# Kernel optimization log

Measured on AMD Instinct MI355X. Metric: run time of the kernel, lower is better.

The kernel has to match this reference:

```python
import jax, jax.numpy as jnp
import numpy as np

B, S, D = 2, 2048, 1024
H, DK, DV = 16, 64, 64
EPS = 1e-5
SQRT_DK = float(np.sqrt(DK))


def setup_inputs() -> dict:
    key = jax.random.key(0)
    ks = jax.random.split(key, 8)
    sc = 0.02
    return {
        "x": jax.random.normal(ks[0], (B, S, D), jnp.float32),
        "Wk": jax.random.normal(ks[1], (D, H * DK), jnp.float32) * sc,
        "bk": jnp.zeros((H * DK,), jnp.float32),
        "Wq": jax.random.normal(ks[2], (D, H * DK), jnp.float32) * sc,
        "bq": jnp.zeros((H * DK,), jnp.float32),
        "Wv": jax.random.normal(ks[3], (D, H * DV), jnp.float32) * sc,
        "bv": jnp.zeros((H * DV,), jnp.float32),
        "Wo": jax.random.normal(ks[4], (H * DV, D), jnp.float32) * sc,
        "bo": jnp.zeros((D,), jnp.float32),
        "gamma": jnp.ones((D,), jnp.float32),
        "beta": jnp.zeros((D,), jnp.float32),
    }


def reference(x, Wk, bk, Wq, bq, Wv, bv, Wo, bo, gamma, beta):
    b, s, d = x.shape
    # NOTE: original torch code reshapes (B, S, H*dk) directly to (B, H, S, dk)
    # without a transpose; we replicate that exact (non-standard) reshape.
    keys = (x @ Wk + bk).reshape(b, H, s, DK)
    queries = (x @ Wq + bq).reshape(b, H, s, DK)
    values = (x @ Wv + bv).reshape(b, H, s, DV)

    scores = jnp.einsum('bhqd,bhkd->bhqk', queries, keys) / SQRT_DK
    causal_mask = jnp.triu(jnp.ones((s, s), bool), k=1)  # True = masked
    scores = jnp.where(causal_mask[None, None], jnp.float32(-1e9), scores)
    attention = jax.nn.softmax(scores, axis=-1)

    context = jnp.einsum('bhqk,bhkd->bhqd', attention, values)
    context = context.reshape(b, s, H * DV)

    out = context @ Wo + bo  # dropout is identity at inference
    out = out + x            # residual connection

    mean = jnp.mean(out, axis=-1, keepdims=True)
    var = jnp.mean(jnp.square(out - mean), axis=-1, keepdims=True)
    return (out - mean) / jnp.sqrt(var + EPS) * gamma + beta
```

## Files before the change

kernel.cpp:

```cpp
#include <hip/hip_runtime.h>


typedef __attribute__((ext_vector_type(8))) __bf16 bf16x8;
typedef __attribute__((ext_vector_type(8))) unsigned short ushort8;
typedef __attribute__((ext_vector_type(4))) float f32x4;

static __device__ __forceinline__ unsigned short f2bf(float f) {
    unsigned u = __builtin_bit_cast(unsigned, f);
    u += 0x7fffu + ((u >> 16) & 1u);
    return (unsigned short)(u >> 16);
}

__global__ __launch_bounds__(256) void cast_kernel(const float* __restrict__ src,
                                                   unsigned short* __restrict__ dst, int n4) {
    int i = blockIdx.x * 256 + threadIdx.x;
    if (i >= n4) return;
    float4 v = ((const float4*)src)[i];
    ushort4 o;
    o.x = f2bf(v.x); o.y = f2bf(v.y); o.z = f2bf(v.z); o.w = f2bf(v.w);
    ((ushort4*)dst)[i] = o;
}

__global__ __launch_bounds__(256) void castT_kernel(const float* __restrict__ src,
                                                    unsigned short* __restrict__ dst) {
    __shared__ __align__(16) unsigned short t[64 * 68];
    const int tid = threadIdx.x;
    const int n0 = blockIdx.x * 64, k0 = blockIdx.y * 64;
    #pragma unroll
    for (int u = 0; u < 4; u++) {
        int e = u * 256 + tid;
        int r = e >> 4, c4 = (e & 15) * 4;
        float4 v = *(const float4*)(src + (k0 + r) * 1024 + n0 + c4);
        ushort4 o;
        o.x = f2bf(v.x); o.y = f2bf(v.y); o.z = f2bf(v.z); o.w = f2bf(v.w);
        *(ushort4*)(t + r * 68 + c4) = o;
    }
    __syncthreads();
    #pragma unroll
    for (int u = 0; u < 4; u++) {
        int e = u * 256 + tid;
        int rn = e >> 4, ck = (e & 15) * 4;
        ushort4 o;
        o.x = t[(ck + 0) * 68 + rn];
        o.y = t[(ck + 1) * 68 + rn];
        o.z = t[(ck + 2) * 68 + rn];
        o.w = t[(ck + 3) * 68 + rn];
        *(ushort4*)(dst + (n0 + rn) * 1024 + k0 + ck) = o;
    }
}

__global__ __launch_bounds__(256) void vtrans_kernel(const unsigned short* __restrict__ V,
                                                     unsigned short* __restrict__ VT) {
    __shared__ __align__(16) unsigned short t[64 * 68];
    const int tid = threadIdx.x;
    const int p0 = blockIdx.x * 64;
    const long base = (long)blockIdx.y * 131072;
    #pragma unroll
    for (int u = 0; u < 2; u++) {
        int e = u * 256 + tid;
        int r = e >> 3, c8 = (e & 7) * 8;
        ushort8 v = *(const ushort8*)(V + base + (long)(p0 + r) * 64 + c8);
        *(ushort8*)(t + r * 68 + c8) = v;
    }
    __syncthreads();
    #pragma unroll
    for (int u = 0; u < 4; u++) {
        int e = u * 256 + tid;
        int dv = e >> 4, pk = (e & 15) * 4;
        ushort4 o;
        o.x = t[(pk + 0) * 68 + dv];
        o.y = t[(pk + 1) * 68 + dv];
        o.z = t[(pk + 2) * 68 + dv];
        o.w = t[(pk + 3) * 68 + dv];
        *(ushort4*)(VT + base + (long)dv * 2048 + p0 + pk) = o;
    }
}

__global__ __launch_bounds__(256, 3) void gemm_kernel(
    const unsigned short* __restrict__ A,
    const unsigned short* __restrict__ Bt,
    const float* __restrict__ b0, const float* __restrict__ b1, const float* __restrict__ b2,
    unsigned short* __restrict__ outQ, unsigned short* __restrict__ outK,
    unsigned short* __restrict__ outV,
    float* __restrict__ outF, const float* __restrict__ resid, int mode)
{
    __shared__ __align__(16) unsigned short As[2][128 * 32];
    __shared__ __align__(16) unsigned short Bs[2][128 * 32];
    const int tid = threadIdx.x;
    const int lane = tid & 63, wave = tid >> 6;
    const int quad = lane >> 4, l16 = lane & 15;
    const int wm = wave >> 1, wn = wave & 1;
    const int row0 = blockIdx.y * 128, n0g = blockIdx.x * 128;

    const int sr = tid >> 2;
    const int sc = (tid & 3) * 8;
    const unsigned short* Ag0 = A + (size_t)(row0 + sr) * 1024 + sc;
    const unsigned short* Ag1 = A + (size_t)(row0 + 64 + sr) * 1024 + sc;
    const unsigned short* Bg0 = Bt + (size_t)(n0g + sr) * 1024 + sc;
    const unsigned short* Bg1 = Bt + (size_t)(n0g + 64 + sr) * 1024 + sc;

    {
        ushort8 a0 = *(const ushort8*)(Ag0);
        ushort8 a1 = *(const ushort8*)(Ag1);
        ushort8 bv0 = *(const ushort8*)(Bg0);
        ushort8 bv1 = *(const ushort8*)(Bg1);
        *(ushort8*)(As[0] + sr * 32 + sc) = a0;
        *(ushort8*)(As[0] + (64 + sr) * 32 + sc) = a1;
        *(ushort8*)(Bs[0] + sr * 32 + sc) = bv0;
        *(ushort8*)(Bs[0] + (64 + sr) * 32 + sc) = bv1;
    }
    __syncthreads();

    f32x4 acc[4][4] = {};
    #pragma unroll 2
    for (int it = 0; it < 32; ++it) {
        const int cur = it & 1;
        ushort8 na0, na1, nb0, nb1;
        if (it < 31) {
            const int k0 = (it + 1) * 32;
            na0 = *(const ushort8*)(Ag0 + k0);
            na1 = *(const ushort8*)(Ag1 + k0);
            nb0 = *(const ushort8*)(Bg0 + k0);
            nb1 = *(const ushort8*)(Bg1 + k0);
        }
        bf16x8 af[4], bfr[4];
        #pragma unroll
        for (int i = 0; i < 4; i++)
            af[i] = *(const bf16x8*)(As[cur] + (wm * 64 + i * 16 + l16) * 32 + quad * 8);
        #pragma unroll
        for (int j = 0; j < 4; j++)
            bfr[j] = *(const bf16x8*)(Bs[cur] + (wn * 64 + j * 16 + l16) * 32 + quad * 8);
        #pragma unroll
        for (int i = 0; i < 4; i++)
            #pragma unroll
            for (int j = 0; j < 4; j++)
                acc[i][j] = __builtin_amdgcn_mfma_f32_16x16x32_bf16(af[i], bfr[j], acc[i][j], 0, 0, 0);
        if (it < 31) {
            const int nxt = cur ^ 1;
            *(ushort8*)(As[nxt] + sr * 32 + sc) = na0;
            *(ushort8*)(As[nxt] + (64 + sr) * 32 + sc) = na1;
            *(ushort8*)(Bs[nxt] + sr * 32 + sc) = nb0;
            *(ushort8*)(Bs[nxt] + (64 + sr) * 32 + sc) = nb1;
            __syncthreads();
        }
    }

    if (mode == 0) {
        const int which = n0g >> 10;
        const float* bp = (which == 0) ? b0 : (which == 1) ? b1 : b2;
        unsigned short* op = (which == 0) ? outQ : (which == 1) ? outK : outV;
        const float scl = (which == 0) ? 0.125f : 1.0f;
        #pragma unroll
        for (int i = 0; i < 4; i++)
            #pragma unroll
            for (int j = 0; j < 4; j++) {
                int c = (n0g + wn * 64 + j * 16 + l16) & 1023;
                float bj = bp[c];
                #pragma unroll
                for (int r = 0; r < 4; r++) {
                    int r_g = row0 + wm * 64 + i * 16 + quad * 4 + r;
                    op[(size_t)r_g * 1024 + c] = f2bf((acc[i][j][r] + bj) * scl);
                }
            }
    } else {
        #pragma unroll
        for (int i = 0; i < 4; i++)
            #pragma unroll
            for (int j = 0; j < 4; j++) {
                int c_g = n0g + wn * 64 + j * 16 + l16;
                float bj = b0[c_g];
                #pragma unroll
                for (int r = 0; r < 4; r++) {
                    int r_g = row0 + wm * 64 + i * 16 + quad * 4 + r;
                    size_t idx = (size_t)r_g * 1024 + c_g;
                    outF[idx] = acc[i][j][r] + bj + resid[idx];
                }
            }
    }
}

__global__ __launch_bounds__(256, 3) void flash_kernel(
    const unsigned short* __restrict__ Q,
    const unsigned short* __restrict__ K,
    const unsigned short* __restrict__ VT,
    unsigned short* __restrict__ Ctx)
{
    __shared__ __align__(16) unsigned short Kt[128 * 72];
    __shared__ __align__(16) unsigned short Vt[64 * 136];
    __shared__ __align__(16) unsigned short Pt[4][16 * 140];
    const int tid = threadIdx.x;
    const int lane = tid & 63, wave = tid >> 6;
    const int quad = lane >> 4, l16 = lane & 15;
    const int qb = 31 - blockIdx.y;
    const int q0 = qb * 64;
    const long base = (long)blockIdx.x * 131072;

    bf16x8 qa[2];
    #pragma unroll
    for (int kk = 0; kk < 2; kk++)
        qa[kk] = *(const bf16x8*)(Q + base + (q0 + wave * 16 + l16) * 64 + kk * 32 + quad * 8);

    f32x4 o[4] = {};
    float l_part[4] = {0.f, 0.f, 0.f, 0.f};
    const int nt = (qb + 2) >> 1;

    #pragma unroll
    for (int u = 0; u < 4; u++) {
        int e = u * 256 + tid;
        int r = e >> 3, c = (e & 7) * 8;
        *(ushort8*)(Kt + r * 72 + c) = *(const ushort8*)(K + base + (long)r * 64 + c);
        int dv = e >> 4, kc = (e & 15) * 8;
        *(ushort8*)(Vt + dv * 136 + kc) = *(const ushort8*)(VT + base + (long)dv * 2048 + kc);
    }
    __syncthreads();

    for (int t = 0; t < nt; t++) {
        ushort8 nk[4], nv[4];
        if (t + 1 < nt) {
            const int k1 = (t + 1) * 128;
            #pragma unroll
            for (int u = 0; u < 4; u++) {
                int e = u * 256 + tid;
                int r = e >> 3, c = (e & 7) * 8;
                nk[u] = *(const ushort8*)(K + base + (long)(k1 + r) * 64 + c);
                int dv = e >> 4, kc = (e & 15) * 8;
                nv[u] = *(const ushort8*)(VT + base + (long)dv * 2048 + k1 + kc);
            }
        }
        const int k0 = t * 128;

        f32x4 s[8];
        #pragma unroll
        for (int c = 0; c < 8; c++) {
            bf16x8 kb0 = *(const bf16x8*)(Kt + (c * 16 + l16) * 72 + quad * 8);
            bf16x8 kb1 = *(const bf16x8*)(Kt + (c * 16 + l16) * 72 + 32 + quad * 8);
            f32x4 a = {};
            a = __builtin_amdgcn_mfma_f32_16x16x32_bf16(qa[0], kb0, a, 0, 0, 0);
            a = __builtin_amdgcn_mfma_f32_16x16x32_bf16(qa[1], kb1, a, 0, 0, 0);
            s[c] = a;
        }
        const bool diag = (t == nt - 1);
        #pragma unroll
        for (int c = 0; c < 8; c++)
            #pragma unroll
            for (int r = 0; r < 4; r++) {
                float p = __expf(s[c][r]);
                if (diag) {
                    int kpos = k0 + c * 16 + l16;
                    int qpos = q0 + wave * 16 + quad * 4 + r;
                    p = (kpos > qpos) ? 0.f : p;
                }
                s[c][r] = p;
            }
        #pragma unroll
        for (int r = 0; r < 4; r++) {
            float t0 = (s[0][r] + s[1][r]) + (s[2][r] + s[3][r]);
            float t1 = (s[4][r] + s[5][r]) + (s[6][r] + s[7][r]);
            l_part[r] += t0 + t1;
        }
        unsigned short* pw = Pt[wave];
        #pragma unroll
        for (int c = 0; c < 8; c++)
            #pragma unroll
            for (int r = 0; r < 4; r++)
                pw[(quad * 4 + r) * 140 + c * 16 + l16] = f2bf(s[c][r]);
        bf16x8 pa[4];
        #pragma unroll
        for (int kk = 0; kk < 4; kk++) {
            const unsigned short* pr = pw + l16 * 140 + kk * 32 + quad * 8;
            ushort4 lo = *(const ushort4*)(pr);
            ushort4 hi = *(const ushort4*)(pr + 4);
            ushort8 u8;
            u8[0] = lo.x; u8[1] = lo.y; u8[2] = lo.z; u8[3] = lo.w;
            u8[4] = hi.x; u8[5] = hi.y; u8[6] = hi.z; u8[7] = hi.w;
            pa[kk] = __builtin_bit_cast(bf16x8, u8);
        }
        #pragma unroll
        for (int c2 = 0; c2 < 4; c2++)
            #pragma unroll
            for (int kk = 0; kk < 4; kk++) {
                bf16x8 vb = *(const bf16x8*)(Vt + (c2 * 16 + l16) * 136 + kk * 32 + quad * 8);
                o[c2] = __builtin_amdgcn_mfma_f32_16x16x32_bf16(pa[kk], vb, o[c2], 0, 0, 0);
            }
        __syncthreads();
        if (t + 1 < nt) {
            #pragma unroll
            for (int u = 0; u < 4; u++) {
                int e = u * 256 + tid;
                int r = e >> 3, c = (e & 7) * 8;
                *(ushort8*)(Kt + r * 72 + c) = nk[u];
                int dv = e >> 4, kc = (e & 15) * 8;
                *(ushort8*)(Vt + dv * 136 + kc) = nv[u];
            }
            __syncthreads();
        }
    }

    #pragma unroll
    for (int r = 0; r < 4; r++) {
        float l = l_part[r];
        #pragma unroll
        for (int off = 1; off < 16; off <<= 1) l += __shfl_xor(l, off, 64);
        l_part[r] = 1.0f / l;
    }
    #pragma unroll
    for (int c2 = 0; c2 < 4; c2++)
        #pragma unroll
        for (int r = 0; r < 4; r++) {
            int row = q0 + wave * 16 + quad * 4 + r;
            Ctx[base + (long)row * 64 + c2 * 16 + l16] = f2bf(o[c2][r] * l_part[r]);
        }
}

__global__ __launch_bounds__(256) void ln_kernel(const float* __restrict__ inp,
                                                 const float* __restrict__ gamma,
                                                 const float* __restrict__ beta,
                                                 float* __restrict__ out)
{
    __shared__ float ssum[4], ssq[4];
    const int row = blockIdx.x;
    const int tid = threadIdx.x;
    float4 v = ((const float4*)(inp + (size_t)row * 1024))[tid];
    float s = v.x + v.y + v.z + v.w;
    float q = v.x * v.x + v.y * v.y + v.z * v.z + v.w * v.w;
    #pragma unroll
    for (int off = 32; off >= 1; off >>= 1) {
        s += __shfl_xor(s, off, 64);
        q += __shfl_xor(q, off, 64);
    }
    if ((tid & 63) == 0) { ssum[tid >> 6] = s; ssq[tid >> 6] = q; }
    __syncthreads();
    float ts = ssum[0] + ssum[1] + ssum[2] + ssum[3];
    float tq = ssq[0] + ssq[1] + ssq[2] + ssq[3];
    float mean = ts * (1.f / 1024.f);
    float var = tq * (1.f / 1024.f) - mean * mean;
    float rinv = rsqrtf(var + 1e-5f);
    float4 g = ((const float4*)gamma)[tid];
    float4 b = ((const float4*)beta)[tid];
    float4 o;
    o.x = (v.x - mean) * rinv * g.x + b.x;
    o.y = (v.y - mean) * rinv * g.y + b.y;
    o.z = (v.z - mean) * rinv * g.z + b.z;
    o.w = (v.w - mean) * rinv * g.w + b.w;
    ((float4*)(out + (size_t)row * 1024))[tid] = o;
}

extern "C" void kernel_launch(void* const* d_in, const int* in_sizes, int n_in,
                              void* d_out, int out_size, void* d_ws, size_t ws_size,
                              hipStream_t stream) {
    const float* x     = (const float*)d_in[0];
    const float* Wk    = (const float*)d_in[1];
    const float* bk    = (const float*)d_in[2];
    const float* Wq    = (const float*)d_in[3];
    const float* bq    = (const float*)d_in[4];
    const float* Wv    = (const float*)d_in[5];
    const float* bv    = (const float*)d_in[6];
    const float* Wo    = (const float*)d_in[7];
    const float* bo    = (const float*)d_in[8];
    const float* gamma = (const float*)d_in[9];
    const float* beta  = (const float*)d_in[10];
    float* out = (float*)d_out;

    char* ws = (char*)d_ws;
    unsigned short* xb    = (unsigned short*)(ws);
    unsigned short* WqkvT = (unsigned short*)(ws + (8ull << 20));
    unsigned short* WoT   = (unsigned short*)(ws + (14ull << 20));
    unsigned short* Qb    = (unsigned short*)(ws + (16ull << 20));
    unsigned short* Kb    = (unsigned short*)(ws + (24ull << 20));
    unsigned short* VbT   = (unsigned short*)(ws + (32ull << 20));
    unsigned short* Cb    = (unsigned short*)(ws + (40ull << 20));
    float* outp           = (float*)(ws + (48ull << 20));
    unsigned short* Vbn   = Cb;

    cast_kernel<<<4096, 256, 0, stream>>>(x, xb, 1048576);
    dim3 tgrid(16, 16);
    castT_kernel<<<tgrid, 256, 0, stream>>>(Wq, WqkvT);
    castT_kernel<<<tgrid, 256, 0, stream>>>(Wk, WqkvT + (1u << 20));
    castT_kernel<<<tgrid, 256, 0, stream>>>(Wv, WqkvT + (2u << 20));
    castT_kernel<<<tgrid, 256, 0, stream>>>(Wo, WoT);

    dim3 qkvgrid(24, 32);
    gemm_kernel<<<qkvgrid, 256, 0, stream>>>(xb, WqkvT, bq, bk, bv,
                                             Qb, Kb, Vbn, nullptr, nullptr, 0);

    dim3 vgrid(32, 32);
    vtrans_kernel<<<vgrid, 256, 0, stream>>>(Vbn, VbT);

    dim3 fgrid(32, 32);
    flash_kernel<<<fgrid, 256, 0, stream>>>(Qb, Kb, VbT, Cb);

    dim3 ogrid(8, 32);
    gemm_kernel<<<ogrid, 256, 0, stream>>>(Cb, WoT, bo, nullptr, nullptr,
                                           nullptr, nullptr, nullptr, outp, x, 1);

    ln_kernel<<<4096, 256, 0, stream>>>(outp, gamma, beta, out);
}
```

Before: 211.7 us.

## Compute transposed scores to feed P directly into 16x16x16 MFMA without LDS

Swaps the operands of the QK^T MFMA so each lane holds score values laid out as the A-operand of a 16x16x16 bf16 MFMA. P then feeds the PV product straight from registers, skipping the per-wave LDS round trip. Score tiles lying entirely above the causal diagonal are skipped, the row-sum reduction is simplified, and launch bounds rise to 4 blocks per CU when the smaller MFMA is available. In exchange the PV product uses twice as many smaller MFMA instructions, which may lower matrix throughput.

```diff
diff --git a/kernel.cpp b/kernel.cpp
--- a/kernel.cpp
+++ b/kernel.cpp
@@ -2,8 +2,33 @@
 
 
 typedef __attribute__((ext_vector_type(8))) __bf16 bf16x8;
+typedef __attribute__((ext_vector_type(4))) __bf16 bf16x4;
 typedef __attribute__((ext_vector_type(8))) unsigned short ushort8;
+typedef __attribute__((ext_vector_type(4))) unsigned short u16x4;
+typedef __attribute__((ext_vector_type(4))) short s16x4;
 typedef __attribute__((ext_vector_type(4))) float f32x4;
+
+#if __has_builtin(__builtin_amdgcn_mfma_f32_16x16x16_bf16)
+#define HAVE_MFMA16 1
+#define MFMA16_NATIVE 1
+#elif __has_builtin(__builtin_amdgcn_mfma_f32_16x16x16bf16_1k)
+#define HAVE_MFMA16 1
+#endif
+
+#if HAVE_MFMA16
+static __device__ __forceinline__ f32x4 mfma16bf(u16x4 a, u16x4 b, f32x4 c) {
+#ifdef MFMA16_NATIVE
+    return __builtin_amdgcn_mfma_f32_16x16x16_bf16(
+        __builtin_bit_cast(bf16x4, a), __builtin_bit_cast(bf16x4, b), c, 0, 0, 0);
+#else
+    return __builtin_amdgcn_mfma_f32_16x16x16bf16_1k(
+        __builtin_bit_cast(s16x4, a), __builtin_bit_cast(s16x4, b), c, 0, 0, 0);
+#endif
+}
+#define FLASH_BOUNDS 4
+#else
+#define FLASH_BOUNDS 3
+#endif
 
 static __device__ __forceinline__ unsigned short f2bf(float f) {
     unsigned u = __builtin_bit_cast(unsigned, f);
@@ -179,15 +204,17 @@
     }
 }
 
-__global__ __launch_bounds__(256, 3) void flash_kernel(
+__global__ __launch_bounds__(256, FLASH_BOUNDS) void flash_kernel(
     const unsigned short* __restrict__ Q,
     const unsigned short* __restrict__ K,
     const unsigned short* __restrict__ VT,
     unsigned short* __restrict__ Ctx)
 {
     __shared__ __align__(16) unsigned short Kt[128 * 72];
-    __shared__ __align__(16) unsigned short Vt[64 * 136];
-    __shared__ __align__(16) unsigned short Pt[4][16 * 140];
+    __shared__ __align__(16) unsigned short Vt[64 * 140];
+#if !HAVE_MFMA16
+    __shared__ __align__(16) unsigned short Pt[4][16 * 136];
+#endif
     const int tid = threadIdx.x;
     const int lane = tid & 63, wave = tid >> 6;
     const int quad = lane >> 4, l16 = lane & 15;
@@ -201,8 +228,9 @@
         qa[kk] = *(const bf16x8*)(Q + base + (q0 + wave * 16 + l16) * 64 + kk * 32 + quad * 8);
 
     f32x4 o[4] = {};
-    float l_part[4] = {0.f, 0.f, 0.f, 0.f};
+    float l_one = 0.f;
     const int nt = (qb + 2) >> 1;
+    const int qpos = q0 + wave * 16 + l16;
 
     #pragma unroll
     for (int u = 0; u < 4; u++) {
@@ -210,7 +238,7 @@
         int r = e >> 3, c = (e & 7) * 8;
         *(ushort8*)(Kt + r * 72 + c) = *(const ushort8*)(K + base + (long)r * 64 + c);
         int dv = e >> 4, kc = (e & 15) * 8;
-        *(ushort8*)(Vt + dv * 136 + kc) = *(const ushort8*)(VT + base + (long)dv * 2048 + kc);
+        *(ushort8*)(Vt + dv * 140 + kc) = *(const ushort8*)(VT + base + (long)dv * 2048 + kc);
     }
     __syncthreads();
 
@@ -228,60 +256,67 @@
             }
         }
         const int k0 = t * 128;
+        const int climit = (q0 + 63 - k0) >> 4;
+        const bool diag = (t == nt - 1);
 
         f32x4 s[8];
         #pragma unroll
         for (int c = 0; c < 8; c++) {
-            bf16x8 kb0 = *(const bf16x8*)(Kt + (c * 16 + l16) * 72 + quad * 8);
-            bf16x8 kb1 = *(const bf16x8*)(Kt + (c * 16 + l16) * 72 + 32 + quad * 8);
-            f32x4 a = {};
-            a = __builtin_amdgcn_mfma_f32_16x16x32_bf16(qa[0], kb0, a, 0, 0, 0);
-            a = __builtin_amdgcn_mfma_f32_16x16x32_bf16(qa[1], kb1, a, 0, 0, 0);
-            s[c] = a;
-        }
-        const bool diag = (t == nt - 1);
-        #pragma unroll
-        for (int c = 0; c < 8; c++)
-            #pragma unroll
-            for (int r = 0; r < 4; r++) {
-                float p = __expf(s[c][r]);
-                if (diag) {
-                    int kpos = k0 + c * 16 + l16;
-                    int qpos = q0 + wave * 16 + quad * 4 + r;
-                    p = (kpos > qpos) ? 0.f : p;
+            if (c <= climit) {
+                bf16x8 kb0 = *(const bf16x8*)(Kt + (c * 16 + l16) * 72 + quad * 8);
+                bf16x8 kb1 = *(const bf16x8*)(Kt + (c * 16 + l16) * 72 + 32 + quad * 8);
+                f32x4 a = {};
+                a = __builtin_amdgcn_mfma_f32_16x16x32_bf16(kb0, qa[0], a, 0, 0, 0);
+                a = __builtin_amdgcn_mfma_f32_16x16x32_bf16(kb1, qa[1], a, 0, 0, 0);
+                #pragma unroll
+                for (int r = 0; r < 4; r++) {
+                    float p = __expf(a[r]);
+                    if (diag) {
+                        int kpos = k0 + c * 16 + quad * 4 + r;
+                        p = (kpos > qpos) ? 0.f : p;
+                    }
+                    a[r] = p;
                 }
-                s[c][r] = p;
-            }
-        #pragma unroll
-        for (int r = 0; r < 4; r++) {
-            float t0 = (s[0][r] + s[1][r]) + (s[2][r] + s[3][r]);
-            float t1 = (s[4][r] + s[5][r]) + (s[6][r] + s[7][r]);
-            l_part[r] += t0 + t1;
-        }
+                s[c] = a;
+                l_one += (a[0] + a[1]) + (a[2] + a[3]);
+            }
+        }
+
+#if HAVE_MFMA16
+        #pragma unroll
+        for (int kg = 0; kg < 8; kg++) {
+            if (kg <= climit) {
+                u16x4 pa;
+                pa[0] = f2bf(s[kg][0]); pa[1] = f2bf(s[kg][1]);
+                pa[2] = f2bf(s[kg][2]); pa[3] = f2bf(s[kg][3]);
+                #pragma unroll
+                for (int c2 = 0; c2 < 4; c2++) {
+                    u16x4 vb = *(const u16x4*)(Vt + (c2 * 16 + l16) * 140 + kg * 16 + quad * 4);
+                    o[c2] = mfma16bf(pa, vb, o[c2]);
+                }
+            }
+        }
+#else
         unsigned short* pw = Pt[wave];
         #pragma unroll
-        for (int c = 0; c < 8; c++)
-            #pragma unroll
-            for (int r = 0; r < 4; r++)
-                pw[(quad * 4 + r) * 140 + c * 16 + l16] = f2bf(s[c][r]);
-        bf16x8 pa[4];
+        for (int c = 0; c < 8; c++) {
+            u16x4 pk4 = {};
+            if (c <= climit) {
+                pk4[0] = f2bf(s[c][0]); pk4[1] = f2bf(s[c][1]);
+                pk4[2] = f2bf(s[c][2]); pk4[3] = f2bf(s[c][3]);
+            }
+            *(u16x4*)(pw + l16 * 136 + c * 16 + quad * 4) = pk4;
+        }
         #pragma unroll
         for (int kk = 0; kk < 4; kk++) {
-            const unsigned short* pr = pw + l16 * 140 + kk * 32 + quad * 8;
-            ushort4 lo = *(const ushort4*)(pr);
-            ushort4 hi = *(const ushort4*)(pr + 4);
-            ushort8 u8;
-            u8[0] = lo.x; u8[1] = lo.y; u8[2] = lo.z; u8[3] = lo.w;
-            u8[4] = hi.x; u8[5] = hi.y; u8[6] = hi.z; u8[7] = hi.w;
-            pa[kk] = __builtin_bit_cast(bf16x8, u8);
-        }
-        #pragma unroll
-        for (int c2 = 0; c2 < 4; c2++)
-            #pragma unroll
-            for (int kk = 0; kk < 4; kk++) {
-                bf16x8 vb = *(const bf16x8*)(Vt + (c2 * 16 + l16) * 136 + kk * 32 + quad * 8);
-                o[c2] = __builtin_amdgcn_mfma_f32_16x16x32_bf16(pa[kk], vb, o[c2], 0, 0, 0);
-            }
+            bf16x8 pa = *(const bf16x8*)(pw + l16 * 136 + kk * 32 + quad * 8);
+            #pragma unroll
+            for (int c2 = 0; c2 < 4; c2++) {
+                bf16x8 vb = *(const bf16x8*)(Vt + (c2 * 16 + l16) * 140 + kk * 32 + quad * 8);
+                o[c2] = __builtin_amdgcn_mfma_f32_16x16x32_bf16(pa, vb, o[c2], 0, 0, 0);
+            }
+        }
+#endif
         __syncthreads();
         if (t + 1 < nt) {
             #pragma unroll
@@ -290,25 +325,24 @@
                 int r = e >> 3, c = (e & 7) * 8;
                 *(ushort8*)(Kt + r * 72 + c) = nk[u];
                 int dv = e >> 4, kc = (e & 15) * 8;
-                *(ushort8*)(Vt + dv * 136 + kc) = nv[u];
+                *(ushort8*)(Vt + dv * 140 + kc) = nv[u];
             }
             __syncthreads();
         }
     }
 
-    #pragma unroll
-    for (int r = 0; r < 4; r++) {
-        float l = l_part[r];
-        #pragma unroll
-        for (int off = 1; off < 16; off <<= 1) l += __shfl_xor(l, off, 64);
-        l_part[r] = 1.0f / l;
-    }
+    l_one += __shfl_xor(l_one, 16, 64);
+    l_one += __shfl_xor(l_one, 32, 64);
+    float rinv[4];
+    #pragma unroll
+    for (int r = 0; r < 4; r++)
+        rinv[r] = 1.0f / __shfl(l_one, quad * 4 + r, 16);
     #pragma unroll
     for (int c2 = 0; c2 < 4; c2++)
         #pragma unroll
         for (int r = 0; r < 4; r++) {
             int row = q0 + wave * 16 + quad * 4 + r;
-            Ctx[base + (long)row * 64 + c2 * 16 + l16] = f2bf(o[c2][r] * l_part[r]);
+            Ctx[base + (long)row * 64 + c2 * 16 + l16] = f2bf(o[c2][r] * rinv[r]);
         }
 }
 
```

Measured after the change: 217.1 us. 1.03x slower.
